# Kernel optimization log

Measured on AMD Instinct MI355X. Metric: run time of the kernel, lower is better.

Reference implementation:

```python
import jax, jax.numpy as jnp
import numpy as np

NUM_HEADS = 4
EPS = 1e-12  # torch F.normalize eps


def _l2norm(t):
    # normalize along last axis, matching torch.nn.functional.normalize
    n = jnp.sqrt(jnp.sum(t * t, axis=-1, keepdims=True))
    return t / jnp.maximum(n, EPS)


def setup_inputs() -> dict:
    key = jax.random.key(0)
    k1, k2 = jax.random.split(key)
    B, N, C = 4, 8192, 768
    x = jax.random.normal(k1, (B, N, C), dtype=jnp.float32)
    W_qkvv = jax.random.normal(k2, (3 * C, C), dtype=jnp.float32) * (C ** -0.5)
    temperature = jnp.ones((NUM_HEADS, 1, 1), dtype=jnp.float32)
    return {"x": x, "W_qkvv": W_qkvv, "temperature": temperature}


def reference(x, W_qkvv, temperature):
    B, N, C = x.shape
    H = NUM_HEADS
    D = C // H
    # qkvv projection: [B,N,3C] -> [3,B,H,N,D]
    qkvv = (x @ W_qkvv.T).reshape(B, N, 3, H, D).transpose(2, 0, 3, 1, 4)
    q, k, v = qkvv[0], qkvv[1], qkvv[2]        # each [B,H,N,D]
    q = jnp.swapaxes(q, -2, -1)                # [B,H,D,N]
    k = jnp.swapaxes(k, -2, -1)                # [B,H,D,N]
    v = jnp.swapaxes(v, -2, -1)                # [B,H,D,N]
    q = _l2norm(q)
    k = _l2norm(k)
    # channel attention scores: [B,H,D,D], temperature broadcast per head
    attn = jnp.einsum('bhdn,bhen->bhde', q, k) * temperature[None]
    attn = jax.nn.softmax(attn, axis=-1)
    # dropout is identity in eval mode
    x_CA = jnp.einsum('bhde,bhen->bhdn', attn, v)   # [B,H,D,N]
    out = x_CA.transpose(0, 3, 1, 2).reshape(B, N, C)
    return out
```

## Files before the change

### kernel.cpp

```cpp
#include <hip/hip_runtime.h>
#include <hip/hip_bf16.h>
#include <cstddef>
#include <cstdint>

#define B_   4
#define N_   8192
#define C_   768
#define H_   4
#define D_   192
#define CQ_  2304
#define M_   32768

typedef __attribute__((ext_vector_type(8))) short short8_t;
typedef __attribute__((ext_vector_type(4))) float f32x4;

typedef const __attribute__((address_space(1))) uint gq_uint;
typedef __attribute__((address_space(3))) uint lds_uint;

__device__ inline ushort f2bf(float f){
  uint u = __float_as_uint(f);
  u += 0x7FFFu + ((u >> 16) & 1u);
  return (ushort)(u >> 16);
}
__device__ inline float bf2f(ushort u){ return __uint_as_float(((uint)u) << 16); }

__global__ __launch_bounds__(256) void cvt_bf16(const float* __restrict__ src,
                                                ushort* __restrict__ dst, int n4){
  int i = blockIdx.x * 256 + threadIdx.x;
  if (i < n4){
    float4 v = ((const float4*)src)[i];
    ushort4 o;
    o.x = f2bf(v.x); o.y = f2bf(v.y); o.z = f2bf(v.z); o.w = f2bf(v.w);
    ((ushort4*)dst)[i] = o;
  }
}

__global__ __launch_bounds__(512, 2) void gemm_qkvv(const ushort* __restrict__ A,
                                                    const ushort* __restrict__ W,
                                                    ushort* __restrict__ Cq,
                                                    float* __restrict__ norm2){
  extern __shared__ ushort lds[];
  const int t = threadIdx.x;
  const int bid = blockIdx.x;
  const int wg  = (bid & 7) * 144 + (bid >> 3);
  const int by = wg / 9, bx = wg % 9;
  const int m0 = by * 256, n0 = bx * 256;
  const int wid = t >> 6, lane = t & 63;
  const int wm = wid >> 2, wn = wid & 3;
  const int lr = lane & 15, lg = lane >> 4;
  const int srow  = lane >> 3;
  const int sslot = (lane & 7) ^ srow;

  f32x4 acc[8][4];
  #pragma unroll
  for (int i = 0; i < 8; ++i)
    #pragma unroll
    for (int j = 0; j < 4; ++j)
      acc[i][j] = (f32x4){0.f, 0.f, 0.f, 0.f};

  #define STAGE(KT, CUR)                                                          \
    do {                                                                          \
      const int k0_ = (KT) * 64;                                                  \
      ushort* bA_ = lds + (CUR) * 32768;                                          \
      ushort* bB_ = bA_ + 16384;                                                  \
      _Pragma("unroll")                                                           \
      for (int i_ = 0; i_ < 4; ++i_){                                             \
        const int r_ = i_ * 64 + wid * 8;                                         \
        __builtin_amdgcn_global_load_lds(                                         \
            (gq_uint*)(const void*)(A + (size_t)(m0 + r_ + srow) * 768 + k0_ + sslot * 8), \
            (lds_uint*)(void*)(bA_ + r_ * 64), 16, 0, 0);                         \
        __builtin_amdgcn_global_load_lds(                                         \
            (gq_uint*)(const void*)(W + (size_t)(n0 + r_ + srow) * 768 + k0_ + sslot * 8), \
            (lds_uint*)(void*)(bB_ + r_ * 64), 16, 0, 0);                         \
      }                                                                           \
    } while (0)

  STAGE(0, 0);
  STAGE(1, 1);
  asm volatile("s_waitcnt vmcnt(8)" ::: "memory");
  __builtin_amdgcn_s_barrier();
  __builtin_amdgcn_sched_barrier(0);

  for (int kt = 0; kt < 12; ++kt){
    const int cur = kt & 1;
    const ushort* bA = lds + cur * 32768;
    const ushort* bB = bA + 16384;

    short8_t af[2][8], bf[2][4];
    #pragma unroll
    for (int kk = 0; kk < 2; ++kk){
      const int sl = ((kk * 4 + lg) ^ (lr & 7)) * 8;
      #pragma unroll
      for (int fm = 0; fm < 8; ++fm)
        af[kk][fm] = *(const short8_t*)(bA + (wm * 128 + fm * 16 + lr) * 64 + sl);
      #pragma unroll
      for (int fn = 0; fn < 4; ++fn)
        bf[kk][fn] = *(const short8_t*)(bB + (wn * 64 + fn * 16 + lr) * 64 + sl);
    }

    __builtin_amdgcn_s_setprio(1);
    #pragma unroll
    for (int fm = 0; fm < 8; ++fm)
      #pragma unroll
      for (int fn = 0; fn < 4; ++fn)
        acc[fm][fn] = __builtin_amdgcn_mfma_f32_16x16x32_bf16(af[0][fm], bf[0][fn], acc[fm][fn], 0, 0, 0);
    __builtin_amdgcn_s_setprio(0);

    asm volatile("s_waitcnt lgkmcnt(0)" ::: "memory");
    __builtin_amdgcn_sched_barrier(0);
    __builtin_amdgcn_s_barrier();
    __builtin_amdgcn_sched_barrier(0);

    if (kt + 2 < 12) STAGE(kt + 2, cur);

    __builtin_amdgcn_s_setprio(1);
    #pragma unroll
    for (int fm = 0; fm < 8; ++fm)
      #pragma unroll
      for (int fn = 0; fn < 4; ++fn)
        acc[fm][fn] = __builtin_amdgcn_mfma_f32_16x16x32_bf16(af[1][fm], bf[1][fn], acc[fm][fn], 0, 0, 0);
    __builtin_amdgcn_s_setprio(0);

    if (kt < 11){
      if (kt + 2 < 12) asm volatile("s_waitcnt vmcnt(8)" ::: "memory");
      else             asm volatile("s_waitcnt vmcnt(0)" ::: "memory");
      __builtin_amdgcn_s_barrier();
      __builtin_amdgcn_sched_barrier(0);
    }
  }
  #undef STAGE

  #pragma unroll
  for (int fm = 0; fm < 8; ++fm)
    #pragma unroll
    for (int fn = 0; fn < 4; ++fn)
      #pragma unroll
      for (int r = 0; r < 4; ++r){
        int m = m0 + wm * 128 + fm * 16 + lg * 4 + r;
        int c = n0 + wn * 64 + fn * 16 + lr;
        Cq[(size_t)m * CQ_ + c] = f2bf(acc[fm][fn][r]);
      }

  if (bx < 6){
    const int b = m0 >> 13;
    #pragma unroll
    for (int fn = 0; fn < 4; ++fn){
      float s = 0.f;
      #pragma unroll
      for (int fm = 0; fm < 8; ++fm)
        #pragma unroll
        for (int r = 0; r < 4; ++r)
          s = fmaf(acc[fm][fn][r], acc[fm][fn][r], s);
      s += __shfl_xor(s, 16);
      s += __shfl_xor(s, 32);
      if (lg == 0)
        atomicAdd(&norm2[b * 1536 + n0 + wn * 64 + fn * 16 + lr], s);
    }
  }
}

__global__ __launch_bounds__(256) void gram_mfma(const ushort* __restrict__ Qk,
                                                 float* __restrict__ Sp){
  const int kc = blockIdx.x;
  const int bh = blockIdx.y;
  const int eh = blockIdx.z;
  const int b = bh >> 2, h = bh & 3;
  __shared__ __align__(16) ushort qs[32][194];
  __shared__ __align__(16) ushort ks[32][98];
  const int t = threadIdx.x;
  const int w = t >> 6, lane = t & 63;
  const int wd = w >> 1, we = w & 1;
  const int lr = lane & 15, lg = lane >> 4;

  f32x4 acc[6][3];
  #pragma unroll
  for (int i = 0; i < 6; ++i)
    #pragma unroll
    for (int j = 0; j < 3; ++j)
      acc[i][j] = (f32x4){0.f, 0.f, 0.f, 0.f};

  const uint* qb = (const uint*)Qk + ((size_t)b * N_ * CQ_ + h * 192) / 2;
  const uint* kb = (const uint*)Qk + ((size_t)b * N_ * CQ_ + 768 + h * 192 + eh * 96) / 2;

  for (int it = 0; it < 32; ++it){
    const int n0 = kc * 1024 + it * 32;
    __syncthreads();
    #pragma unroll
    for (int u = 0; u < 3; ++u){
      int g = u * 256 + t;
      int row = g / 24, c4 = g % 24;
      uint4 v = ((const uint4*)(qb + (size_t)(n0 + row) * 1152))[c4];
      uint* dst = (uint*)&qs[row][8 * c4];
      dst[0] = v.x; dst[1] = v.y; dst[2] = v.z; dst[3] = v.w;
    }
    #pragma unroll
    for (int u = 0; u < 3; ++u){
      int g = u * 256 + t;
      int row = g / 24, c2 = g % 24;
      uint2 v = ((const uint2*)(kb + (size_t)(n0 + row) * 1152))[c2];
      uint* dst = (uint*)&ks[row][4 * c2];
      dst[0] = v.x; dst[1] = v.y;
    }
    __syncthreads();
    union { uint u[4]; short8_t v; } af[6], bf[3];
    #pragma unroll
    for (int i = 0; i < 6; ++i){
      int d = wd * 96 + i * 16 + lr;
      #pragma unroll
      for (int p = 0; p < 4; ++p)
        af[i].u[p] = (uint)qs[lg*8 + 2*p][d] | ((uint)qs[lg*8 + 2*p + 1][d] << 16);
    }
    #pragma unroll
    for (int j = 0; j < 3; ++j){
      int e = we * 48 + j * 16 + lr;
      #pragma unroll
      for (int p = 0; p < 4; ++p)
        bf[j].u[p] = (uint)ks[lg*8 + 2*p][e] | ((uint)ks[lg*8 + 2*p + 1][e] << 16);
    }
    #pragma unroll
    for (int i = 0; i < 6; ++i)
      #pragma unroll
      for (int j = 0; j < 3; ++j)
        acc[i][j] = __builtin_amdgcn_mfma_f32_16x16x32_bf16(af[i].v, bf[j].v, acc[i][j], 0, 0, 0);
  }
  float* base = Sp + (size_t)(kc * 16 + bh) * 192 * 192;
  #pragma unroll
  for (int i = 0; i < 6; ++i)
    #pragma unroll
    for (int j = 0; j < 3; ++j)
      #pragma unroll
      for (int r = 0; r < 4; ++r){
        int d = wd * 96 + i * 16 + lg * 4 + r;
        int e = eh * 96 + we * 48 + j * 16 + lr;
        base[(size_t)d * 192 + e] = acc[i][j][r];
      }
}

__global__ __launch_bounds__(256) void softmax_k(const float* __restrict__ Sp,
                                                 const float* __restrict__ norm2,
                                                 const float* __restrict__ temp,
                                                 ushort* __restrict__ attn){
  const int wid  = blockIdx.x * 4 + (threadIdx.x >> 6);
  const int lane = threadIdx.x & 63;
  const int bh = wid / 192, d = wid % 192;
  const int b = bh >> 2, h = bh & 3;
  const float nq = sqrtf(norm2[b*1536 + h*192 + d]);
  const float sc = temp[h] / fmaxf(nq, 1e-12f);
  const float* Sr = Sp + ((size_t)bh * 192 + d) * 192;
  float l[3];
  #pragma unroll
  for (int u = 0; u < 3; ++u){
    int e = lane + u * 64;
    float s = 0.f;
    #pragma unroll
    for (int kc = 0; kc < 8; ++kc)
      s += Sr[(size_t)kc * (16*192*192) + e];
    float nk = sqrtf(norm2[b*1536 + 768 + h*192 + e]);
    l[u] = s * sc / fmaxf(nk, 1e-12f);
  }
  float m = fmaxf(l[0], fmaxf(l[1], l[2]));
  #pragma unroll
  for (int off = 32; off; off >>= 1) m = fmaxf(m, __shfl_xor(m, off));
  float p[3], s = 0.f;
  #pragma unroll
  for (int u = 0; u < 3; ++u){ p[u] = expf(l[u] - m); s += p[u]; }
  #pragma unroll
  for (int off = 32; off; off >>= 1) s += __shfl_xor(s, off);
  float inv = 1.f / s;
  ushort* ar = attn + ((size_t)bh * 192 + d) * 192;
  #pragma unroll
  for (int u = 0; u < 3; ++u) ar[lane + u*64] = f2bf(p[u] * inv);
}

__global__ __launch_bounds__(256) void out_gemm(const ushort* __restrict__ Q,
                                                const ushort* __restrict__ attn,
                                                float* __restrict__ out){
  const int bh = blockIdx.y;
  const int b = bh >> 2, h = bh & 3;
  const int n0 = blockIdx.x * 128;
  const int t = threadIdx.x, w = t >> 6, lane = t & 63;
  const int wn = w & 1, wd = w >> 1;
  const int lr = lane & 15, lg = lane >> 4;
  f32x4 acc[4][6];
  #pragma unroll
  for (int i = 0; i < 4; ++i)
    #pragma unroll
    for (int j = 0; j < 6; ++j)
      acc[i][j] = (f32x4){0.f, 0.f, 0.f, 0.f};

  const ushort* Vbase = Q + 1536 + h * 192;
  const ushort* Abase = attn + (size_t)bh * 192 * 192;

  #pragma unroll
  for (int kk = 0; kk < 6; ++kk){
    const int e = kk * 32 + lg * 8;
    short8_t av[4], bv[6];
    #pragma unroll
    for (int f = 0; f < 4; ++f){
      int n = n0 + wn*64 + f*16 + lr;
      av[f] = *(const short8_t*)(Vbase + (size_t)(b*N_ + n) * CQ_ + e);
    }
    #pragma unroll
    for (int f = 0; f < 6; ++f){
      int d = wd*96 + f*16 + lr;
      bv[f] = *(const short8_t*)(Abase + d * 192 + e);
    }
    #pragma unroll
    for (int i = 0; i < 4; ++i)
      #pragma unroll
      for (int j = 0; j < 6; ++j)
        acc[i][j] = __builtin_amdgcn_mfma_f32_16x16x32_bf16(av[i], bv[j], acc[i][j], 0, 0, 0);
  }
  #pragma unroll
  for (int i = 0; i < 4; ++i)
    #pragma unroll
    for (int j = 0; j < 6; ++j)
      #pragma unroll
      for (int r = 0; r < 4; ++r){
        int n = n0 + wn*64 + i*16 + lg*4 + r;
        int c = h*192 + wd*96 + j*16 + lr;
        out[(size_t)(b*N_ + n) * 768 + c] = acc[i][j][r];
      }
}

extern "C" void kernel_launch(void* const* d_in, const int* in_sizes, int n_in,
                              void* d_out, int out_size, void* d_ws, size_t ws_size,
                              hipStream_t stream){
  const float* x    = (const float*)d_in[0];
  const float* Wq   = (const float*)d_in[1];
  const float* temp = (const float*)d_in[2];
  float* out = (float*)d_out;
  char* ws = (char*)d_ws;

  ushort* xb    = (ushort*)(ws + 0);
  float*  S_part= (float*)(ws + 0);
  ushort* attn  = (ushort*)(ws + 37748736);
  ushort* Wb    = (ushort*)(ws + 50331648);
  ushort* qkvv  = (ushort*)(ws + 53870592);
  float*  norm2 = (float*)(ws + 204865536);

  static_assert(sizeof(ushort) == 2, "");
  hipFuncSetAttribute((const void*)gemm_qkvv,
                      hipFuncAttributeMaxDynamicSharedMemorySize, 131072);

  hipMemsetAsync(norm2, 0, 24576, stream);

  cvt_bf16<<<6291456/256, 256, 0, stream>>>(x,  xb, 6291456);
  cvt_bf16<<<442368/256,  256, 0, stream>>>(Wq, Wb, 442368);

  gemm_qkvv<<<1152, 512, 131072, stream>>>(xb, Wb, qkvv, norm2);

  gram_mfma<<<dim3(8, 16, 2), 256, 0, stream>>>(qkvv, S_part);
  softmax_k<<<768, 256, 0, stream>>>(S_part, norm2, temp, attn);
  out_gemm<<<dim3(64, 16), 256, 0, stream>>>(qkvv, attn, out);
}
```

Baseline: 250.6 us.

## Restructure QKV GEMM mainloop into quadrant-interleaved half-tile load/compute pipeline

```diff
diff --git a/kernel.cpp b/kernel.cpp
--- a/kernel.cpp
+++ b/kernel.cpp
@@ -58,103 +58,123 @@
     for (int j = 0; j < 4; ++j)
       acc[i][j] = (f32x4){0.f, 0.f, 0.f, 0.f};
 
-  #define STAGE(KT, CUR)                                                          \
-    do {                                                                          \
-      const int k0_ = (KT) * 64;                                                  \
-      ushort* bA_ = lds + (CUR) * 32768;                                          \
-      ushort* bB_ = bA_ + 16384;                                                  \
-      _Pragma("unroll")                                                           \
-      for (int i_ = 0; i_ < 4; ++i_){                                             \
-        const int r_ = i_ * 64 + wid * 8;                                         \
-        __builtin_amdgcn_global_load_lds(                                         \
-            (gq_uint*)(const void*)(A + (size_t)(m0 + r_ + srow) * 768 + k0_ + sslot * 8), \
-            (lds_uint*)(void*)(bA_ + r_ * 64), 16, 0, 0);                         \
-        __builtin_amdgcn_global_load_lds(                                         \
-            (gq_uint*)(const void*)(W + (size_t)(n0 + r_ + srow) * 768 + k0_ + sslot * 8), \
-            (lds_uint*)(void*)(bB_ + r_ * 64), 16, 0, 0);                         \
-      }                                                                           \
+  #define STAGE_HALF(GPTR, G0, KT, LBASE, HALF)                                 \
+    do {                                                                        \
+      _Pragma("unroll")                                                         \
+      for (int rnd_ = 0; rnd_ < 2; ++rnd_){                                     \
+        const int row_ = (HALF) * 128 + rnd_ * 64 + wid * 8;                    \
+        __builtin_amdgcn_global_load_lds(                                       \
+            (gq_uint*)(const void*)((GPTR) + (size_t)((G0) + row_ + srow) * 768 \
+                                    + (KT) * 64 + sslot * 8),                   \
+            (lds_uint*)(void*)((LBASE) + row_ * 64), 16, 0, 0);                 \
+      }                                                                         \
     } while (0)
 
-  STAGE(0, 0);
-  STAGE(1, 1);
-  asm volatile("s_waitcnt vmcnt(8)" ::: "memory");
+  #define RD_A(DST, MH)                                                         \
+    _Pragma("unroll") for (int kk = 0; kk < 2; ++kk){                           \
+      const int sl = ((kk * 4 + lg) ^ (lr & 7)) * 8;                            \
+      _Pragma("unroll") for (int fm = 0; fm < 4; ++fm)                          \
+        DST[kk][fm] = *(const short8_t*)(bA + ((MH)*128 + wm*64 + fm*16 + lr)*64 + sl); }
+
+  #define RD_B(DST, NH)                                                         \
+    _Pragma("unroll") for (int kk = 0; kk < 2; ++kk){                           \
+      const int sl = ((kk * 4 + lg) ^ (lr & 7)) * 8;                            \
+      _Pragma("unroll") for (int fl = 0; fl < 2; ++fl)                          \
+        DST[kk][fl] = *(const short8_t*)(bB + ((NH)*128 + wn*32 + fl*16 + lr)*64 + sl); }
+
+  #define MM(AR, BR, IO, JO)                                                    \
+    __builtin_amdgcn_s_setprio(1);                                              \
+    _Pragma("unroll") for (int kk = 0; kk < 2; ++kk)                            \
+    _Pragma("unroll") for (int fm = 0; fm < 4; ++fm)                            \
+    _Pragma("unroll") for (int fl = 0; fl < 2; ++fl)                            \
+      acc[(IO)+fm][(JO)+fl] = __builtin_amdgcn_mfma_f32_16x16x32_bf16(          \
+          AR[kk][fm], BR[kk][fl], acc[(IO)+fm][(JO)+fl], 0, 0, 0);              \
+    __builtin_amdgcn_s_setprio(0);
+
+  #define WAITP(N)                                                              \
+    asm volatile("s_waitcnt vmcnt(" #N ")" ::: "memory");                       \
+    __builtin_amdgcn_s_barrier();                                               \
+    asm volatile("s_waitcnt lgkmcnt(0)" ::: "memory");                          \
+    __builtin_amdgcn_sched_barrier(0);
+
+  STAGE_HALF(A, m0, 0, lds,         0);
+  STAGE_HALF(A, m0, 0, lds,         1);
+  STAGE_HALF(W, n0, 0, lds + 16384, 0);
+  STAGE_HALF(W, n0, 0, lds + 16384, 1);
+  asm volatile("s_waitcnt vmcnt(0)" ::: "memory");
   __builtin_amdgcn_s_barrier();
   __builtin_amdgcn_sched_barrier(0);
 
-  for (int kt = 0; kt < 12; ++kt){
-    const int cur = kt & 1;
-    const ushort* bA = lds + cur * 32768;
+  short8_t a0[2][4], a1[2][4], bf0[2][2], bf1[2][2];
+
+  #pragma unroll 2
+  for (int kt = 0; kt < 11; ++kt){
+    const ushort* bA = lds + (kt & 1) * 32768;
     const ushort* bB = bA + 16384;
-
-    short8_t af[2][8], bf[2][4];
-    #pragma unroll
-    for (int kk = 0; kk < 2; ++kk){
-      const int sl = ((kk * 4 + lg) ^ (lr & 7)) * 8;
-      #pragma unroll
-      for (int fm = 0; fm < 8; ++fm)
-        af[kk][fm] = *(const short8_t*)(bA + (wm * 128 + fm * 16 + lr) * 64 + sl);
-      #pragma unroll
-      for (int fn = 0; fn < 4; ++fn)
-        bf[kk][fn] = *(const short8_t*)(bB + (wn * 64 + fn * 16 + lr) * 64 + sl);
-    }
-
-    __builtin_amdgcn_s_setprio(1);
-    #pragma unroll
-    for (int fm = 0; fm < 8; ++fm)
-      #pragma unroll
-      for (int fn = 0; fn < 4; ++fn)
-        acc[fm][fn] = __builtin_amdgcn_mfma_f32_16x16x32_bf16(af[0][fm], bf[0][fn], acc[fm][fn], 0, 0, 0);
-    __builtin_amdgcn_s_setprio(0);
-
+    ushort* nA = lds + ((kt + 1) & 1) * 32768;
+    ushort* nB = nA + 16384;
+    RD_A(a0, 0); RD_B(bf0, 0);
+    STAGE_HALF(A, m0, kt + 1, nA, 0);
+    WAITP(4);
+    MM(a0, bf0, 0, 0);
+    RD_A(a1, 1);
+    STAGE_HALF(W, n0, kt + 1, nB, 0);
+    WAITP(4);
+    MM(a1, bf0, 4, 0);
+    RD_B(bf1, 1);
+    STAGE_HALF(A, m0, kt + 1, nA, 1);
+    WAITP(4);
+    MM(a1, bf1, 4, 2);
+    STAGE_HALF(W, n0, kt + 1, nB, 1);
+    WAITP(4);
+    MM(a0, bf1, 0, 2);
+  }
+  {
+    const ushort* bA = lds + 32768;
+    const ushort* bB = bA + 16384;
+    RD_A(a0, 0); RD_B(bf0, 0);
+    WAITP(2);
+    MM(a0, bf0, 0, 0);
+    RD_A(a1, 1);
+    WAITP(0);
+    MM(a1, bf0, 4, 0);
+    RD_B(bf1, 1);
     asm volatile("s_waitcnt lgkmcnt(0)" ::: "memory");
     __builtin_amdgcn_sched_barrier(0);
-    __builtin_amdgcn_s_barrier();
-    __builtin_amdgcn_sched_barrier(0);
-
-    if (kt + 2 < 12) STAGE(kt + 2, cur);
-
-    __builtin_amdgcn_s_setprio(1);
-    #pragma unroll
-    for (int fm = 0; fm < 8; ++fm)
-      #pragma unroll
-      for (int fn = 0; fn < 4; ++fn)
-        acc[fm][fn] = __builtin_amdgcn_mfma_f32_16x16x32_bf16(af[1][fm], bf[1][fn], acc[fm][fn], 0, 0, 0);
-    __builtin_amdgcn_s_setprio(0);
-
-    if (kt < 11){
-      if (kt + 2 < 12) asm volatile("s_waitcnt vmcnt(8)" ::: "memory");
-      else             asm volatile("s_waitcnt vmcnt(0)" ::: "memory");
-      __builtin_amdgcn_s_barrier();
-      __builtin_amdgcn_sched_barrier(0);
-    }
-  }
-  #undef STAGE
-
-  #pragma unroll
-  for (int fm = 0; fm < 8; ++fm)
-    #pragma unroll
-    for (int fn = 0; fn < 4; ++fn)
+    MM(a1, bf1, 4, 2);
+    MM(a0, bf1, 0, 2);
+  }
+  #undef STAGE_HALF
+  #undef RD_A
+  #undef RD_B
+  #undef MM
+  #undef WAITP
+
+  #pragma unroll
+  for (int i = 0; i < 8; ++i)
+    #pragma unroll
+    for (int j = 0; j < 4; ++j)
       #pragma unroll
       for (int r = 0; r < 4; ++r){
-        int m = m0 + wm * 128 + fm * 16 + lg * 4 + r;
-        int c = n0 + wn * 64 + fn * 16 + lr;
-        Cq[(size_t)m * CQ_ + c] = f2bf(acc[fm][fn][r]);
+        int m = m0 + (i >> 2) * 128 + wm * 64 + (i & 3) * 16 + lg * 4 + r;
+        int c = n0 + (j >> 1) * 128 + wn * 32 + (j & 1) * 16 + lr;
+        Cq[(size_t)m * CQ_ + c] = f2bf(acc[i][j][r]);
       }
 
   if (bx < 6){
     const int b = m0 >> 13;
     #pragma unroll
-    for (int fn = 0; fn < 4; ++fn){
+    for (int j = 0; j < 4; ++j){
       float s = 0.f;
       #pragma unroll
-      for (int fm = 0; fm < 8; ++fm)
+      for (int i = 0; i < 8; ++i)
         #pragma unroll
         for (int r = 0; r < 4; ++r)
-          s = fmaf(acc[fm][fn][r], acc[fm][fn][r], s);
+          s = fmaf(acc[i][j][r], acc[i][j][r], s);
       s += __shfl_xor(s, 16);
       s += __shfl_xor(s, 32);
       if (lg == 0)
-        atomicAdd(&norm2[b * 1536 + n0 + wn * 64 + fn * 16 + lr], s);
+        atomicAdd(&norm2[b * 1536 + n0 + (j >> 1) * 128 + wn * 32 + (j & 1) * 16 + lr], s);
     }
   }
 }
```

After: 248.7 us. No clear change (-0.7%).
